# Optimization experiments

Hardware: AMD Instinct MI355X
Metric: run time of the kernel (lower is better)

## Reference

```python
import jax, jax.numpy as jnp
import numpy as np

OUT = 7      # roi_align output_size
RATIO = 2    # fixed sampling_ratio (torchvision default -1 is adaptive; fixed 2 used for jit-ability)
IMG = 518    # image size (DINOv2 patch 14 -> 37x37 feature grid)


def setup_inputs() -> dict:
    key = jax.random.key(0)
    ks = jax.random.split(key, 12)
    B, N, C, H, W = 4, 512, 256, 37, 37
    NUM_CLASSES = 91
    f0 = jax.random.normal(ks[0], (B, C, H, W), jnp.float32)
    f1 = jax.random.normal(ks[1], (B, C, H, W), jnp.float32)
    f2 = jax.random.normal(ks[2], (B, C, H, W), jnp.float32)
    f3 = jax.random.normal(ks[3], (B, C, H, W), jnp.float32)
    # proposals in image coords so areas span all 4 level buckets (32^2..128^2+)
    cx = jax.random.uniform(ks[4], (B, N)) * IMG
    cy = jax.random.uniform(ks[5], (B, N)) * IMG
    bw = jax.random.uniform(ks[6], (B, N)) * 248.0 + 8.0
    bh = jax.random.uniform(ks[7], (B, N)) * 248.0 + 8.0
    x1 = jnp.maximum(cx - 0.5 * bw, 0.0)
    y1 = jnp.maximum(cy - 0.5 * bh, 0.0)
    x2 = jnp.minimum(cx + 0.5 * bw, float(IMG))
    y2 = jnp.minimum(cy + 0.5 * bh, float(IMG))
    proposals = jnp.stack([x1, y1, x2, y2], axis=-1)  # [B,N,4]
    D = C * OUT * OUT  # 12544
    w1 = jax.random.normal(ks[8], (D, 1024), jnp.float32) * 0.02
    b1 = jnp.zeros((1024,), jnp.float32)
    w2 = jax.random.normal(ks[9], (1024, 1024), jnp.float32) * 0.02
    b2 = jnp.zeros((1024,), jnp.float32)
    wc = jax.random.normal(ks[10], (1024, NUM_CLASSES), jnp.float32) * 0.02
    bc = jnp.zeros((NUM_CLASSES,), jnp.float32)
    wb = jax.random.normal(ks[11], (1024, 4), jnp.float32) * 0.02
    bb = jnp.zeros((4,), jnp.float32)
    return {"f0": f0, "f1": f1, "f2": f2, "f3": f3, "proposals": proposals,
            "w1": w1, "b1": b1, "w2": w2, "b2": b2,
            "wc": wc, "bc": bc, "wb": wb, "bb": bb}


def _multilevel_roi_align(f0, f1, f2, f3, proposals):
    B, C, H, W = f0.shape
    N = proposals.shape[1]
    P = OUT * RATIO * OUT * RATIO
    # levels stacked along spatial axis: [B, C, 4*H*W]
    feats_cat = jnp.stack([f0, f1, f2, f3], axis=2).reshape(B, C, 4 * H * W)
    bw = proposals[..., 2] - proposals[..., 0]
    bh = proposals[..., 3] - proposals[..., 1]
    area = bw * bh
    # area-based FPN level: <32^2->0, <64^2->1, <128^2->2, else 3
    lvl = ((area >= 32.0 ** 2).astype(jnp.int32)
           + (area >= 64.0 ** 2).astype(jnp.int32)
           + (area >= 128.0 ** 2).astype(jnp.int32))  # [B,N]
    # roi_align, spatial_scale=1.0, aligned=True
    x1 = proposals[..., 0] - 0.5
    y1 = proposals[..., 1] - 0.5
    bin_w = bw / OUT
    bin_h = bh / OUT
    offs = jnp.arange(OUT, dtype=jnp.float32)[:, None] + (jnp.arange(RATIO, dtype=jnp.float32) + 0.5)[None, :] / RATIO  # [7,2]
    ys = y1[..., None, None] + offs * bin_h[..., None, None]  # [B,N,7,2]
    xs = x1[..., None, None] + offs * bin_w[..., None, None]  # [B,N,7,2]
    y = ys[..., :, :, None, None]  # [B,N,7,2,1,1]
    x = xs[..., None, None, :, :]  # [B,N,1,1,7,2]
    valid = ((y >= -1.0) & (y <= H) & (x >= -1.0) & (x <= W)).astype(f0.dtype)
    yc = jnp.clip(y, 0.0, H - 1.0)
    xc = jnp.clip(x, 0.0, W - 1.0)
    y0f = jnp.floor(yc)
    x0f = jnp.floor(xc)
    y0 = y0f.astype(jnp.int32)
    x0 = x0f.astype(jnp.int32)
    y1i = jnp.minimum(y0 + 1, H - 1)
    x1i = jnp.minimum(x0 + 1, W - 1)
    ly = yc - y0f
    lx = xc - x0f
    hy = 1.0 - ly
    hx = 1.0 - lx
    base = (lvl * (H * W))[:, :, None, None, None, None]
    shp = (B, N, OUT, RATIO, OUT, RATIO)

    def gather(yi, xi):
        idx = jnp.broadcast_to(base + yi * W + xi, shp).reshape(B, N * P)
        return jax.vmap(lambda fb, ib: jnp.take(fb, ib, axis=1))(feats_cat, idx)  # [B,C,N*P]

    def wflat(w):
        return jnp.broadcast_to(w * valid, shp).reshape(B, 1, N * P)

    acc = (wflat(hy * hx) * gather(y0, x0)
           + wflat(hy * lx) * gather(y0, x1i)
           + wflat(ly * hx) * gather(y1i, x0)
           + wflat(ly * lx) * gather(y1i, x1i))
    roi = acc.reshape(B, C, N, OUT, RATIO, OUT, RATIO).sum(axis=(4, 6)) / (RATIO * RATIO)
    return roi.transpose(0, 2, 1, 3, 4)  # [B,N,C,7,7]


def reference(f0, f1, f2, f3, proposals, w1, b1, w2, b2, wc, bc, wb, bb):
    B, N = proposals.shape[0], proposals.shape[1]
    roi = _multilevel_roi_align(f0, f1, f2, f3, proposals)  # [B,N,C,7,7]
    flat = roi.reshape(B * N, -1)  # torch flatten order matches [C,7,7]
    h1 = jax.nn.relu(flat @ w1 + b1)
    h2 = jax.nn.relu(h1 @ w2 + b2)
    scores = (h2 @ wc + bc).reshape(B, N, -1)
    bbox_deltas = (h2 @ wb + bb).reshape(B, N, 4)
    return scores, bbox_deltas
```

## Files before the change

### kernel.cpp

```cpp
#include <hip/hip_runtime.h>
#include <hip/hip_bf16.h>
#include <stdint.h>

#define FH 37
#define FW 37
#define FC 256
#define NB 4
#define NP 512
#define BNT (NB*NP)
#define KDIM (FC*49)
#define HID 1024
#define NHEAD 95
#define CAP 256

typedef __bf16 bf16x8 __attribute__((ext_vector_type(8)));
typedef float  f32x4  __attribute__((ext_vector_type(4)));

__global__ __launch_bounds__(256) void k_init(uint4* __restrict__ Ahi4,
                                              uint4* __restrict__ Alo4,
                                              int* __restrict__ count,
                                              float* __restrict__ h2c_raw) {
  int bid = blockIdx.x;
  if (bid < 1568) {
    int i = bid * 256 + threadIdx.x;
    uint4 z = {0, 0, 0, 0};
    Ahi4[i] = z;
    Alo4[i] = z;
  } else {
    int t = threadIdx.x;
    #pragma unroll
    for (int j = 0; j < 4; ++j) h2c_raw[t + j * 256] = 0.f;
    if (t == 0) *count = 0;
  }
}

__global__ __launch_bounds__(256) void k_transpose(const float* __restrict__ f0,
                                                   const float* __restrict__ f1,
                                                   const float* __restrict__ f2,
                                                   const float* __restrict__ f3,
                                                   float* __restrict__ ft) {
  __shared__ float tile[32][33];
  int bl = blockIdx.z;
  int b = bl >> 2, l = bl & 3;
  const float* src = (l == 0 ? f0 : l == 1 ? f1 : l == 2 ? f2 : f3) + (size_t)b * FC * FH * FW;
  int yx0 = blockIdx.x * 32;
  int c0  = blockIdx.y * 32;
  int tx = threadIdx.x;
  int ty = threadIdx.y;
  #pragma unroll
  for (int i = 0; i < 32; i += 8) {
    int c  = c0 + ty + i;
    int yx = yx0 + tx;
    float v = (yx < FH * FW) ? src[(size_t)c * (FH * FW) + yx] : 0.f;
    tile[ty + i][tx] = v;
  }
  __syncthreads();
  #pragma unroll
  for (int i = 0; i < 32; i += 8) {
    int yx = yx0 + ty + i;
    int c  = c0 + tx;
    if (yx < FH * FW)
      ft[((size_t)bl * (FH * FW) + yx) * FC + c] = tile[tx][ty + i];
  }
}

__global__ __launch_bounds__(256) void k_compact(const float* __restrict__ props,
                                                 int* __restrict__ count,
                                                 int* __restrict__ list) {
  int bn = blockIdx.x * 256 + threadIdx.x;
  float px1 = props[(size_t)bn * 4 + 0];
  float py1 = props[(size_t)bn * 4 + 1];
  float px2 = props[(size_t)bn * 4 + 2];
  float py2 = props[(size_t)bn * 4 + 3];
  float bw = px2 - px1, bh = py2 - py1;
  float X1 = px1 - 0.5f, Y1 = py1 - 0.5f;
  float binw = bw * (1.f / 7.f), binh = bh * (1.f / 7.f);
  float sy0 = Y1 + ((float)0 * 0.5f + 0.25f) * binh;
  float sx0 = X1 + ((float)0 * 0.5f + 0.25f) * binw;
  bool active = (sy0 <= 37.f) && (sx0 <= 37.f);
  if (active) {
    int s = atomicAdd(count, 1);
    if (s < CAP) list[s] = bn;
  }
}

__global__ __launch_bounds__(256) void k_roi(const float* __restrict__ ft,
                                             const float* __restrict__ props,
                                             const int* __restrict__ count,
                                             const int* __restrict__ list,
                                             __hip_bfloat16* __restrict__ Ahi,
                                             __hip_bfloat16* __restrict__ Alo) {
  __shared__ int   s_idx[28][4];
  __shared__ float s_w[28][4];
  int s = blockIdx.x;
  int cnt = min(*count, CAP);
  if (s >= cnt) return;
  int bn = list[s];
  int b = bn >> 9;
  int oy = blockIdx.y;
  int t = threadIdx.x;
  if (t < 28) {
    float px1 = props[(size_t)bn * 4 + 0];
    float py1 = props[(size_t)bn * 4 + 1];
    float px2 = props[(size_t)bn * 4 + 2];
    float py2 = props[(size_t)bn * 4 + 3];
    float bw = px2 - px1, bh = py2 - py1;
    float area = bw * bh;
    int lvl = (area >= 1024.f) + (area >= 4096.f) + (area >= 16384.f);
    float X1 = px1 - 0.5f, Y1 = py1 - 0.5f;
    float binw = bw * (1.f / 7.f), binh = bh * (1.f / 7.f);
    int ry = t / 14, ix = t % 14;
    int iy = oy * 2 + ry;
    float sy = Y1 + ((float)iy * 0.5f + 0.25f) * binh;
    float sx = X1 + ((float)ix * 0.5f + 0.25f) * binw;
    float valid = (sy >= -1.f && sy <= 37.f && sx >= -1.f && sx <= 37.f) ? 0.25f : 0.f;
    float yc = fminf(fmaxf(sy, 0.f), 36.f);
    float xc = fminf(fmaxf(sx, 0.f), 36.f);
    float y0f = floorf(yc), x0f = floorf(xc);
    int y0 = (int)y0f, x0 = (int)x0f;
    int y1i = min(y0 + 1, 36), x1i = min(x0 + 1, 36);
    float ly = yc - y0f, lx = xc - x0f;
    float hy = 1.f - ly, hx = 1.f - lx;
    int base = ((b * 4 + lvl) * (FH * FW)) * FC;
    s_idx[t][0] = base + (y0 * FW + x0) * FC;
    s_idx[t][1] = base + (y0 * FW + x1i) * FC;
    s_idx[t][2] = base + (y1i * FW + x0) * FC;
    s_idx[t][3] = base + (y1i * FW + x1i) * FC;
    s_w[t][0] = hy * hx * valid;
    s_w[t][1] = hy * lx * valid;
    s_w[t][2] = ly * hx * valid;
    s_w[t][3] = ly * lx * valid;
  }
  __syncthreads();
  int c = t;
  size_t outbase = (size_t)s * KDIM;
  for (int ox = 0; ox < 7; ++ox) {
    float acc = 0.f;
    #pragma unroll
    for (int ry = 0; ry < 2; ++ry) {
      #pragma unroll
      for (int rx = 0; rx < 2; ++rx) {
        int sp = ry * 14 + ox * 2 + rx;
        #pragma unroll
        for (int tap = 0; tap < 4; ++tap) {
          float wt = s_w[sp][tap];
          if (wt != 0.f) acc += wt * ft[s_idx[sp][tap] + c];
        }
      }
    }
    int p = oy * 7 + ox;
    __hip_bfloat16 h = __float2bfloat16(acc);
    Ahi[outbase + p * FC + c] = h;
    Alo[outbase + p * FC + c] = __float2bfloat16(acc - __bfloat162float(h));
  }
}

__global__ __launch_bounds__(256) void k_w1(const float* __restrict__ w1,
                                            __hip_bfloat16* __restrict__ Whi,
                                            __hip_bfloat16* __restrict__ Wlo) {
  __shared__ float tile[64][65];
  int p  = blockIdx.x;
  int c0 = blockIdx.y * 64;
  int n0 = blockIdx.z * 64;
  int t = threadIdx.x;
  int tl = t & 63, th = t >> 6;
  #pragma unroll
  for (int i = 0; i < 16; ++i) {
    int r = i * 4 + th;
    tile[r][tl] = w1[((size_t)(c0 + r) * 49 + p) * HID + n0 + tl];
  }
  __syncthreads();
  #pragma unroll
  for (int i = 0; i < 16; ++i) {
    int r = i * 4 + th;
    float v = tile[tl][r];
    __hip_bfloat16 h = __float2bfloat16(v);
    size_t o = (size_t)(n0 + r) * KDIM + p * FC + c0 + tl;
    Whi[o] = h;
    Wlo[o] = __float2bfloat16(v - __bfloat162float(h));
  }
}

__global__ __launch_bounds__(256) void k_w2(const float* __restrict__ w2,
                                            __hip_bfloat16* __restrict__ Whi,
                                            __hip_bfloat16* __restrict__ Wlo) {
  __shared__ float tile[64][65];
  int k0 = blockIdx.x * 64;
  int n0 = blockIdx.y * 64;
  int t = threadIdx.x;
  int tl = t & 63, th = t >> 6;
  #pragma unroll
  for (int i = 0; i < 16; ++i) {
    int r = i * 4 + th;
    tile[r][tl] = w2[(size_t)(k0 + r) * HID + n0 + tl];
  }
  __syncthreads();
  #pragma unroll
  for (int i = 0; i < 16; ++i) {
    int r = i * 4 + th;
    float v = tile[tl][r];
    __hip_bfloat16 h = __float2bfloat16(v);
    size_t o = (size_t)(n0 + r) * HID + k0 + tl;
    Whi[o] = h;
    Wlo[o] = __float2bfloat16(v - __bfloat162float(h));
  }
}

__global__ __launch_bounds__(256) void k_wcb(const float* __restrict__ wc,
                                             const float* __restrict__ bc,
                                             const float* __restrict__ wb,
                                             const float* __restrict__ bb,
                                             float* __restrict__ wcbT,
                                             float* __restrict__ bcb) {
  int j = blockIdx.x;
  int t = threadIdx.x;
  for (int k = t; k < HID; k += 256) {
    float v = (j < 91) ? wc[(size_t)k * 91 + j] : wb[(size_t)k * 4 + (j - 91)];
    wcbT[(size_t)j * HID + k] = v;
  }
  if (t == 0) bcb[j] = (j < 91) ? bc[j] : bb[j - 91];
}

__global__ __launch_bounds__(256) void k_h2c(const float* __restrict__ w2,
                                             const float* __restrict__ b1,
                                             float* __restrict__ h2c_raw) {
  int n = blockIdx.x * 256 + threadIdx.x;
  int k0 = blockIdx.y * 64;
  float acc = 0.f;
  for (int k = k0; k < k0 + 64; ++k) {
    float h = fmaxf(b1[k], 0.f);
    acc += h * w2[(size_t)k * HID + n];
  }
  atomicAdd(&h2c_raw[n], acc);
}

__global__ __launch_bounds__(256) void k_outc(const float* __restrict__ h2c_raw,
                                              const float* __restrict__ b2,
                                              const float* __restrict__ wcbT,
                                              const float* __restrict__ bcb,
                                              float* __restrict__ outc) {
  __shared__ float red[4];
  int j = blockIdx.x;
  int t = threadIdx.x;
  float acc = 0.f;
  for (int n = t; n < HID; n += 256) {
    float h = fmaxf(b2[n] + h2c_raw[n], 0.f);
    acc += h * wcbT[(size_t)j * HID + n];
  }
  #pragma unroll
  for (int o = 32; o; o >>= 1) acc += __shfl_down(acc, o, 64);
  if ((t & 63) == 0) red[t >> 6] = acc;
  __syncthreads();
  if (t == 0) outc[j] = bcb[j] + red[0] + red[1] + red[2] + red[3];
}

__global__ __launch_bounds__(256) void k_fill(const float* __restrict__ outc,
                                              float* __restrict__ out) {
  int i = blockIdx.x * 256 + threadIdx.x;
  const int SC = BNT * 91;
  if (i < SC) out[i] = outc[i % 91];
  else {
    int r = i - SC;
    if (r < BNT * 4) out[SC + r] = outc[91 + (r & 3)];
  }
}

__global__ __launch_bounds__(256) void k_gemm(const __hip_bfloat16* __restrict__ Ahi,
                                              const __hip_bfloat16* __restrict__ Alo,
                                              const __hip_bfloat16* __restrict__ Bhi,
                                              const __hip_bfloat16* __restrict__ Blo,
                                              float* __restrict__ part,
                                              const int* __restrict__ countPtr,
                                              int Mm, int Kt, int Nn, int kChunk) {
  int cnt = min(*countPtr, CAP);
  if (blockIdx.x * 128 >= cnt) return;
  __shared__ char lds[32768];
  int t = threadIdx.x, lane = t & 63, wave = t >> 6;
  int m0 = blockIdx.x * 128, n0 = blockIdx.y * 128;
  int kStart = blockIdx.z * kChunk;

  f32x4 acc[4][4];
  #pragma unroll
  for (int m = 0; m < 4; ++m)
    #pragma unroll
    for (int n = 0; n < 4; ++n)
      acc[m][n] = (f32x4){0.f, 0.f, 0.f, 0.f};

  const __hip_bfloat16* srcs[4] = {
      Ahi + (size_t)m0 * Kt, Alo + (size_t)m0 * Kt,
      Bhi + (size_t)n0 * Kt, Blo + (size_t)n0 * Kt};

  int wm = (wave >> 1) * 64, wn = (wave & 1) * 64;
  int rsel = lane & 15;
  int ksel = (lane >> 4) * 16;

  for (int kk = 0; kk < kChunk; kk += 32) {
    int k0 = kStart + kk;
    #pragma unroll
    for (int tile = 0; tile < 4; ++tile) {
      #pragma unroll
      for (int i = 0; i < 2; ++i) {
        int seg = wave * 2 + i;
        int idx = seg * 64 + lane;
        int row = idx >> 2, col = idx & 3;
        const char* g = (const char*)(srcs[tile] + (size_t)row * Kt + k0 + col * 8);
        char* l = lds + tile * 8192 + seg * 1024;
        __builtin_amdgcn_global_load_lds((const unsigned int __attribute__((address_space(1)))*)g,
                                         (unsigned int __attribute__((address_space(3)))*)l,
                                         16, 0, 0);
      }
    }
    __syncthreads();
    bf16x8 ah[4], al_[4], bh[4], bl_[4];
    #pragma unroll
    for (int m = 0; m < 4; ++m) {
      int off = (wm + m * 16 + rsel) * 64 + ksel;
      ah[m]  = *(const bf16x8*)(lds + off);
      al_[m] = *(const bf16x8*)(lds + 8192 + off);
    }
    #pragma unroll
    for (int n = 0; n < 4; ++n) {
      int off = (wn + n * 16 + rsel) * 64 + ksel;
      bh[n]  = *(const bf16x8*)(lds + 16384 + off);
      bl_[n] = *(const bf16x8*)(lds + 24576 + off);
    }
    #pragma unroll
    for (int m = 0; m < 4; ++m)
      #pragma unroll
      for (int n = 0; n < 4; ++n) {
        acc[m][n] = __builtin_amdgcn_mfma_f32_16x16x32_bf16(ah[m],  bh[n],  acc[m][n], 0, 0, 0);
        acc[m][n] = __builtin_amdgcn_mfma_f32_16x16x32_bf16(ah[m],  bl_[n], acc[m][n], 0, 0, 0);
        acc[m][n] = __builtin_amdgcn_mfma_f32_16x16x32_bf16(al_[m], bh[n],  acc[m][n], 0, 0, 0);
      }
    __syncthreads();
  }

  float* pbase = part + (size_t)blockIdx.z * Mm * Nn;
  #pragma unroll
  for (int m = 0; m < 4; ++m)
    #pragma unroll
    for (int n = 0; n < 4; ++n) {
      int row = m0 + wm + m * 16 + (lane >> 4) * 4;
      int col = n0 + wn + n * 16 + (lane & 15);
      #pragma unroll
      for (int r = 0; r < 4; ++r)
        pbase[(size_t)(row + r) * Nn + col] = acc[m][n][r];
    }
}

template <bool SPLIT_OUT>
__global__ __launch_bounds__(256) void k_reduce(const float* __restrict__ part,
                                                const float* __restrict__ bias,
                                                int Mm, int Nn, int S,
                                                __hip_bfloat16* __restrict__ Hhi,
                                                __hip_bfloat16* __restrict__ Hlo,
                                                float* __restrict__ Hf) {
  size_t i = (size_t)blockIdx.x * 256 + threadIdx.x;
  size_t tot = (size_t)Mm * Nn;
  if (i >= tot) return;
  int col = (int)(i % Nn);
  float a = bias[col];
  for (int s = 0; s < S; ++s) a += part[(size_t)s * tot + i];
  a = fmaxf(a, 0.f);
  if (SPLIT_OUT) {
    __hip_bfloat16 h = __float2bfloat16(a);
    Hhi[i] = h;
    Hlo[i] = __float2bfloat16(a - __bfloat162float(h));
  } else {
    Hf[i] = a;
  }
}

__global__ __launch_bounds__(128) void k_head(const float* __restrict__ h2,
                                              const float* __restrict__ wcbT,
                                              const float* __restrict__ bcb,
                                              const int* __restrict__ count,
                                              const int* __restrict__ list,
                                              float* __restrict__ out) {
  __shared__ float row[HID];
  int s = blockIdx.x;
  int cnt = min(*count, CAP);
  if (s >= cnt) return;
  int bn = list[s];
  int t = threadIdx.x;
  const float4* hr = (const float4*)(h2 + (size_t)s * HID);
  for (int i = t; i < HID / 4; i += 128) ((float4*)row)[i] = hr[i];
  __syncthreads();
  if (t < NHEAD) {
    const float4* w4 = (const float4*)(wcbT + (size_t)t * HID);
    const float4* r4 = (const float4*)row;
    float acc = bcb[t];
    #pragma unroll 4
    for (int k = 0; k < HID / 4; ++k) {
      float4 a = r4[k], b = w4[k];
      acc += a.x * b.x + a.y * b.y + a.z * b.z + a.w * b.w;
    }
    if (t < 91) out[(size_t)bn * 91 + t] = acc;
    else        out[(size_t)BNT * 91 + (size_t)bn * 4 + (t - 91)] = acc;
  }
}

extern "C" void kernel_launch(void* const* d_in, const int* in_sizes, int n_in,
                              void* d_out, int out_size, void* d_ws, size_t ws_size,
                              hipStream_t stream) {
  const float* f0    = (const float*)d_in[0];
  const float* f1    = (const float*)d_in[1];
  const float* f2    = (const float*)d_in[2];
  const float* f3    = (const float*)d_in[3];
  const float* props = (const float*)d_in[4];
  const float* w1    = (const float*)d_in[5];
  const float* b1    = (const float*)d_in[6];
  const float* w2    = (const float*)d_in[7];
  const float* b2    = (const float*)d_in[8];
  const float* wc    = (const float*)d_in[9];
  const float* bc    = (const float*)d_in[10];
  const float* wb    = (const float*)d_in[11];
  const float* bb    = (const float*)d_in[12];
  float* out = (float*)d_out;

  char* ws = (char*)d_ws;
  size_t off = 0;
  auto alloc = [&](size_t bytes) -> char* {
    char* p = ws + off;
    off += (bytes + 255) & ~(size_t)255;
    return p;
  };
  float*          ft    = (float*)         alloc((size_t)16 * FH * FW * FC * 4);
  __hip_bfloat16* Ahi   = (__hip_bfloat16*)alloc((size_t)CAP * KDIM * 2);
  __hip_bfloat16* Alo   = (__hip_bfloat16*)alloc((size_t)CAP * KDIM * 2);
  __hip_bfloat16* W1hi  = (__hip_bfloat16*)alloc((size_t)HID * KDIM * 2);
  __hip_bfloat16* W1lo  = (__hip_bfloat16*)alloc((size_t)HID * KDIM * 2);
  __hip_bfloat16* W2hi  = (__hip_bfloat16*)alloc((size_t)HID * HID * 2);
  __hip_bfloat16* W2lo  = (__hip_bfloat16*)alloc((size_t)HID * HID * 2);
  float*          wcbT  = (float*)         alloc((size_t)96 * HID * 4);
  float*          bcb   = (float*)         alloc(96 * 4);
  float*          part  = (float*)         alloc((size_t)14 * CAP * HID * 4);
  __hip_bfloat16* H1hi  = (__hip_bfloat16*)alloc((size_t)CAP * HID * 2);
  __hip_bfloat16* H1lo  = (__hip_bfloat16*)alloc((size_t)CAP * HID * 2);
  float*          h2    = (float*)         alloc((size_t)CAP * HID * 4);
  int*            count = (int*)           alloc(256);
  int*            list  = (int*)           alloc(CAP * 4);
  float*          h2cr  = (float*)         alloc(HID * 4);
  float*          outc  = (float*)         alloc(NHEAD * 4);
  (void)ws_size; (void)in_sizes; (void)n_in; (void)out_size;

  k_init<<<1569, 256, 0, stream>>>((uint4*)Ahi, (uint4*)Alo, count, h2cr);
  k_transpose<<<dim3(43, 8, 16), dim3(32, 8), 0, stream>>>(f0, f1, f2, f3, ft);
  k_compact<<<8, 256, 0, stream>>>(props, count, list);
  k_roi<<<dim3(CAP, 7), 256, 0, stream>>>(ft, props, count, list, Ahi, Alo);
  k_w1<<<dim3(49, 4, 16), 256, 0, stream>>>(w1, W1hi, W1lo);
  k_w2<<<dim3(16, 16), 256, 0, stream>>>(w2, W2hi, W2lo);
  k_wcb<<<NHEAD, 256, 0, stream>>>(wc, bc, wb, bb, wcbT, bcb);
  k_h2c<<<dim3(4, 16), 256, 0, stream>>>(w2, b1, h2cr);
  k_outc<<<NHEAD, 256, 0, stream>>>(h2cr, b2, wcbT, bcb, outc);
  k_fill<<<760, 256, 0, stream>>>(outc, out);

  k_gemm<<<dim3(CAP / 128, 8, 14), 256, 0, stream>>>(Ahi, Alo, W1hi, W1lo, part, count,
                                                     CAP, KDIM, HID, 896);
  k_reduce<true><<<(CAP * HID + 255) / 256, 256, 0, stream>>>(part, b1, CAP, HID, 14,
                                                              H1hi, H1lo, nullptr);
  k_gemm<<<dim3(CAP / 128, 8, 4), 256, 0, stream>>>(H1hi, H1lo, W2hi, W2lo, part, count,
                                                    CAP, HID, HID, 256);
  k_reduce<false><<<(CAP * HID + 255) / 256, 256, 0, stream>>>(part, b2, CAP, HID, 4,
                                                               nullptr, nullptr, h2);
  k_head<<<CAP, 128, 0, stream>>>(h2, wcbT, bcb, count, list, out);
}
```

Before: 286.3 us.

## Fuse fp32 weight bf16 hi/lo split into a double-buffered GEMM

Removes the per-call preprocessing kernels that converted w1, w2 and the head weights into transposed bf16 hi/lo copies. The GEMM now reads fp32 weights directly, with a K-index reorder for w1's layout, and splits them into hi/lo on the fly into swizzled LDS. It also double-buffers A and B with K=64 stages and doubles the split-K factor. The head and constant-path kernels now read the original weights, the A-buffer zeroing kernel is replaced by a small memset, and the reduces skip rows beyond the valid count. This trades extra conversion ALU work inside the GEMM, and a larger LDS footprint at one block per CU, for eliminating roughly a hundred megabytes of weight write and re-read traffic.

```diff
diff --git a/kernel.cpp b/kernel.cpp
--- a/kernel.cpp
+++ b/kernel.cpp
@@ -15,24 +15,6 @@
 
 typedef __bf16 bf16x8 __attribute__((ext_vector_type(8)));
 typedef float  f32x4  __attribute__((ext_vector_type(4)));
-
-__global__ __launch_bounds__(256) void k_init(uint4* __restrict__ Ahi4,
-                                              uint4* __restrict__ Alo4,
-                                              int* __restrict__ count,
-                                              float* __restrict__ h2c_raw) {
-  int bid = blockIdx.x;
-  if (bid < 1568) {
-    int i = bid * 256 + threadIdx.x;
-    uint4 z = {0, 0, 0, 0};
-    Ahi4[i] = z;
-    Alo4[i] = z;
-  } else {
-    int t = threadIdx.x;
-    #pragma unroll
-    for (int j = 0; j < 4; ++j) h2c_raw[t + j * 256] = 0.f;
-    if (t == 0) *count = 0;
-  }
-}
 
 __global__ __launch_bounds__(256) void k_transpose(const float* __restrict__ f0,
                                                    const float* __restrict__ f1,
@@ -155,129 +137,24 @@
   }
 }
 
-__global__ __launch_bounds__(256) void k_w1(const float* __restrict__ w1,
-                                            __hip_bfloat16* __restrict__ Whi,
-                                            __hip_bfloat16* __restrict__ Wlo) {
-  __shared__ float tile[64][65];
-  int p  = blockIdx.x;
-  int c0 = blockIdx.y * 64;
-  int n0 = blockIdx.z * 64;
-  int t = threadIdx.x;
-  int tl = t & 63, th = t >> 6;
-  #pragma unroll
-  for (int i = 0; i < 16; ++i) {
-    int r = i * 4 + th;
-    tile[r][tl] = w1[((size_t)(c0 + r) * 49 + p) * HID + n0 + tl];
-  }
-  __syncthreads();
-  #pragma unroll
-  for (int i = 0; i < 16; ++i) {
-    int r = i * 4 + th;
-    float v = tile[tl][r];
-    __hip_bfloat16 h = __float2bfloat16(v);
-    size_t o = (size_t)(n0 + r) * KDIM + p * FC + c0 + tl;
-    Whi[o] = h;
-    Wlo[o] = __float2bfloat16(v - __bfloat162float(h));
-  }
-}
-
-__global__ __launch_bounds__(256) void k_w2(const float* __restrict__ w2,
-                                            __hip_bfloat16* __restrict__ Whi,
-                                            __hip_bfloat16* __restrict__ Wlo) {
-  __shared__ float tile[64][65];
-  int k0 = blockIdx.x * 64;
-  int n0 = blockIdx.y * 64;
-  int t = threadIdx.x;
-  int tl = t & 63, th = t >> 6;
-  #pragma unroll
-  for (int i = 0; i < 16; ++i) {
-    int r = i * 4 + th;
-    tile[r][tl] = w2[(size_t)(k0 + r) * HID + n0 + tl];
-  }
-  __syncthreads();
-  #pragma unroll
-  for (int i = 0; i < 16; ++i) {
-    int r = i * 4 + th;
-    float v = tile[tl][r];
-    __hip_bfloat16 h = __float2bfloat16(v);
-    size_t o = (size_t)(n0 + r) * HID + k0 + tl;
-    Whi[o] = h;
-    Wlo[o] = __float2bfloat16(v - __bfloat162float(h));
-  }
-}
-
-__global__ __launch_bounds__(256) void k_wcb(const float* __restrict__ wc,
-                                             const float* __restrict__ bc,
-                                             const float* __restrict__ wb,
-                                             const float* __restrict__ bb,
-                                             float* __restrict__ wcbT,
-                                             float* __restrict__ bcb) {
-  int j = blockIdx.x;
-  int t = threadIdx.x;
-  for (int k = t; k < HID; k += 256) {
-    float v = (j < 91) ? wc[(size_t)k * 91 + j] : wb[(size_t)k * 4 + (j - 91)];
-    wcbT[(size_t)j * HID + k] = v;
-  }
-  if (t == 0) bcb[j] = (j < 91) ? bc[j] : bb[j - 91];
-}
-
-__global__ __launch_bounds__(256) void k_h2c(const float* __restrict__ w2,
-                                             const float* __restrict__ b1,
-                                             float* __restrict__ h2c_raw) {
-  int n = blockIdx.x * 256 + threadIdx.x;
-  int k0 = blockIdx.y * 64;
-  float acc = 0.f;
-  for (int k = k0; k < k0 + 64; ++k) {
-    float h = fmaxf(b1[k], 0.f);
-    acc += h * w2[(size_t)k * HID + n];
-  }
-  atomicAdd(&h2c_raw[n], acc);
-}
-
-__global__ __launch_bounds__(256) void k_outc(const float* __restrict__ h2c_raw,
-                                              const float* __restrict__ b2,
-                                              const float* __restrict__ wcbT,
-                                              const float* __restrict__ bcb,
-                                              float* __restrict__ outc) {
-  __shared__ float red[4];
-  int j = blockIdx.x;
-  int t = threadIdx.x;
-  float acc = 0.f;
-  for (int n = t; n < HID; n += 256) {
-    float h = fmaxf(b2[n] + h2c_raw[n], 0.f);
-    acc += h * wcbT[(size_t)j * HID + n];
-  }
-  #pragma unroll
-  for (int o = 32; o; o >>= 1) acc += __shfl_down(acc, o, 64);
-  if ((t & 63) == 0) red[t >> 6] = acc;
-  __syncthreads();
-  if (t == 0) outc[j] = bcb[j] + red[0] + red[1] + red[2] + red[3];
-}
-
-__global__ __launch_bounds__(256) void k_fill(const float* __restrict__ outc,
-                                              float* __restrict__ out) {
-  int i = blockIdx.x * 256 + threadIdx.x;
-  const int SC = BNT * 91;
-  if (i < SC) out[i] = outc[i % 91];
-  else {
-    int r = i - SC;
-    if (r < BNT * 4) out[SC + r] = outc[91 + (r & 3)];
-  }
-}
-
-__global__ __launch_bounds__(256) void k_gemm(const __hip_bfloat16* __restrict__ Ahi,
-                                              const __hip_bfloat16* __restrict__ Alo,
-                                              const __hip_bfloat16* __restrict__ Bhi,
-                                              const __hip_bfloat16* __restrict__ Blo,
-                                              float* __restrict__ part,
-                                              const int* __restrict__ countPtr,
-                                              int Mm, int Kt, int Nn, int kChunk) {
+__global__ __launch_bounds__(256, 1) void k_gemm_fused(
+    const __hip_bfloat16* __restrict__ Ahi,
+    const __hip_bfloat16* __restrict__ Alo,
+    const float* __restrict__ Wf,
+    float* __restrict__ part,
+    const int* __restrict__ countPtr,
+    int Kt, int kChunk, int reorder) {
   int cnt = min(*countPtr, CAP);
-  if (blockIdx.x * 128 >= cnt) return;
-  __shared__ char lds[32768];
-  int t = threadIdx.x, lane = t & 63, wave = t >> 6;
-  int m0 = blockIdx.x * 128, n0 = blockIdx.y * 128;
-  int kStart = blockIdx.z * kChunk;
+  if ((int)blockIdx.x * 128 >= cnt) return;
+  __shared__ __align__(16) char lds[131072];
+  const int t = threadIdx.x, lane = t & 63, wave = t >> 6;
+  const int m0 = blockIdx.x * 128, n0 = blockIdx.y * 128;
+  const int kStart = blockIdx.z * kChunk;
+  const int niters = kChunk >> 6;
+
+  const int bn = t & 127;
+  const int bkq = t >> 7;
+  const size_t rs = reorder ? (size_t)49 * HID : (size_t)HID;
 
   f32x4 acc[4][4];
   #pragma unroll
@@ -286,79 +163,132 @@
     for (int n = 0; n < 4; ++n)
       acc[m][n] = (f32x4){0.f, 0.f, 0.f, 0.f};
 
-  const __hip_bfloat16* srcs[4] = {
-      Ahi + (size_t)m0 * Kt, Alo + (size_t)m0 * Kt,
-      Bhi + (size_t)n0 * Kt, Blo + (size_t)n0 * Kt};
-
-  int wm = (wave >> 1) * 64, wn = (wave & 1) * 64;
-  int rsel = lane & 15;
-  int ksel = (lane >> 4) * 16;
-
-  for (int kk = 0; kk < kChunk; kk += 32) {
-    int k0 = kStart + kk;
-    #pragma unroll
-    for (int tile = 0; tile < 4; ++tile) {
-      #pragma unroll
-      for (int i = 0; i < 2; ++i) {
-        int seg = wave * 2 + i;
-        int idx = seg * 64 + lane;
-        int row = idx >> 2, col = idx & 3;
-        const char* g = (const char*)(srcs[tile] + (size_t)row * Kt + k0 + col * 8);
-        char* l = lds + tile * 8192 + seg * 1024;
+  float v[32];
+
+  auto stageA = [&](int buf, int k0) {
+    #pragma unroll
+    for (int pl = 0; pl < 2; ++pl) {
+      const __hip_bfloat16* src = pl ? Alo : Ahi;
+      #pragma unroll
+      for (int i = 0; i < 4; ++i) {
+        int seg = wave * 4 + i;
+        int row = seg * 8 + (lane >> 3);
+        int chunk = (lane & 7) ^ (row & 7);
+        const char* g = (const char*)(src + (size_t)(m0 + row) * Kt + k0 + chunk * 8);
+        char* l = lds + buf * 65536 + pl * 16384 + seg * 1024;
         __builtin_amdgcn_global_load_lds((const unsigned int __attribute__((address_space(1)))*)g,
                                          (unsigned int __attribute__((address_space(3)))*)l,
                                          16, 0, 0);
       }
     }
+  };
+
+  auto stageBload = [&](int k0) {
+    size_t rb = reorder ? (size_t)((k0 & 255) * 49 + (k0 >> 8)) : (size_t)k0;
+    const float* p = Wf + rb * HID + (size_t)bkq * 32 * rs + n0 + bn;
+    #pragma unroll
+    for (int j = 0; j < 32; ++j) v[j] = p[(size_t)j * rs];
+  };
+
+  auto stageBwrite = [&](int buf) {
+    char* bh = lds + buf * 65536 + 32768;
+    char* bl = lds + buf * 65536 + 49152;
+    #pragma unroll
+    for (int s = 0; s < 4; ++s) {
+      bf16x8 hv, lv;
+      #pragma unroll
+      for (int e = 0; e < 8; ++e) {
+        float f = v[s * 8 + e];
+        __hip_bfloat16 h = __float2bfloat16(f);
+        float fr = f - __bfloat162float(h);
+        __hip_bfloat16 l2 = __float2bfloat16(fr);
+        hv[e] = *reinterpret_cast<__bf16*>(&h);
+        lv[e] = *reinterpret_cast<__bf16*>(&l2);
+      }
+      int off = bn * 128 + (((bkq * 4 + s) ^ (bn & 7)) << 4);
+      *(bf16x8*)(bh + off) = hv;
+      *(bf16x8*)(bl + off) = lv;
+    }
+  };
+
+  const int wm = (wave >> 1) * 64, wn = (wave & 1) * 64;
+  const int rsel = lane & 15, q = lane >> 4;
+
+  auto compute = [&](int buf) {
+    const char* base = lds + buf * 65536;
+    #pragma unroll
+    for (int kk = 0; kk < 2; ++kk) {
+      bf16x8 ah[4], al_[4], bh[4], bl_[4];
+      #pragma unroll
+      for (int m = 0; m < 4; ++m) {
+        int row = wm + m * 16 + rsel;
+        int off = row * 128 + (((kk * 4 + q) ^ (row & 7)) << 4);
+        ah[m]  = *(const bf16x8*)(base + off);
+        al_[m] = *(const bf16x8*)(base + 16384 + off);
+      }
+      #pragma unroll
+      for (int n = 0; n < 4; ++n) {
+        int col = wn + n * 16 + rsel;
+        int off = col * 128 + (((kk * 4 + q) ^ (col & 7)) << 4);
+        bh[n]  = *(const bf16x8*)(base + 32768 + off);
+        bl_[n] = *(const bf16x8*)(base + 49152 + off);
+      }
+      #pragma unroll
+      for (int m = 0; m < 4; ++m)
+        #pragma unroll
+        for (int n = 0; n < 4; ++n) {
+          acc[m][n] = __builtin_amdgcn_mfma_f32_16x16x32_bf16(ah[m],  bh[n],  acc[m][n], 0, 0, 0);
+          acc[m][n] = __builtin_amdgcn_mfma_f32_16x16x32_bf16(ah[m],  bl_[n], acc[m][n], 0, 0, 0);
+          acc[m][n] = __builtin_amdgcn_mfma_f32_16x16x32_bf16(al_[m], bh[n],  acc[m][n], 0, 0, 0);
+        }
+    }
+  };
+
+  stageBload(kStart);
+  stageA(0, kStart);
+  stageBwrite(0);
+  __syncthreads();
+
+  int cur = 0;
+  for (int it = 0; it < niters; ++it) {
+    int k1 = kStart + (it + 1) * 64;
+    bool havenext = (it + 1 < niters);
+    if (havenext) {
+      stageBload(k1);
+      stageA(cur ^ 1, k1);
+    }
+    compute(cur);
+    if (havenext) stageBwrite(cur ^ 1);
     __syncthreads();
-    bf16x8 ah[4], al_[4], bh[4], bl_[4];
-    #pragma unroll
-    for (int m = 0; m < 4; ++m) {
-      int off = (wm + m * 16 + rsel) * 64 + ksel;
-      ah[m]  = *(const bf16x8*)(lds + off);
-      al_[m] = *(const bf16x8*)(lds + 8192 + off);
-    }
-    #pragma unroll
-    for (int n = 0; n < 4; ++n) {
-      int off = (wn + n * 16 + rsel) * 64 + ksel;
-      bh[n]  = *(const bf16x8*)(lds + 16384 + off);
-      bl_[n] = *(const bf16x8*)(lds + 24576 + off);
-    }
-    #pragma unroll
-    for (int m = 0; m < 4; ++m)
-      #pragma unroll
-      for (int n = 0; n < 4; ++n) {
-        acc[m][n] = __builtin_amdgcn_mfma_f32_16x16x32_bf16(ah[m],  bh[n],  acc[m][n], 0, 0, 0);
-        acc[m][n] = __builtin_amdgcn_mfma_f32_16x16x32_bf16(ah[m],  bl_[n], acc[m][n], 0, 0, 0);
-        acc[m][n] = __builtin_amdgcn_mfma_f32_16x16x32_bf16(al_[m], bh[n],  acc[m][n], 0, 0, 0);
-      }
-    __syncthreads();
-  }
-
-  float* pbase = part + (size_t)blockIdx.z * Mm * Nn;
+    cur ^= 1;
+  }
+
+  float* pbase = part + (size_t)blockIdx.z * (CAP * HID);
   #pragma unroll
   for (int m = 0; m < 4; ++m)
     #pragma unroll
     for (int n = 0; n < 4; ++n) {
-      int row = m0 + wm + m * 16 + (lane >> 4) * 4;
-      int col = n0 + wn + n * 16 + (lane & 15);
+      int row = m0 + wm + m * 16 + q * 4;
+      int col = n0 + wn + n * 16 + rsel;
       #pragma unroll
       for (int r = 0; r < 4; ++r)
-        pbase[(size_t)(row + r) * Nn + col] = acc[m][n][r];
+        pbase[(size_t)(row + r) * HID + col] = acc[m][n][r];
     }
 }
 
 template <bool SPLIT_OUT>
 __global__ __launch_bounds__(256) void k_reduce(const float* __restrict__ part,
                                                 const float* __restrict__ bias,
-                                                int Mm, int Nn, int S,
+                                                const int* __restrict__ countPtr,
+                                                int S,
                                                 __hip_bfloat16* __restrict__ Hhi,
                                                 __hip_bfloat16* __restrict__ Hlo,
                                                 float* __restrict__ Hf) {
+  int cnt = min(*countPtr, CAP);
+  if ((int)(blockIdx.x >> 2) >= cnt) return;
   size_t i = (size_t)blockIdx.x * 256 + threadIdx.x;
-  size_t tot = (size_t)Mm * Nn;
-  if (i >= tot) return;
-  int col = (int)(i % Nn);
+  const size_t tot = (size_t)CAP * HID;
+  int col = (int)(i & (HID - 1));
   float a = bias[col];
   for (int s = 0; s < S; ++s) a += part[(size_t)s * tot + i];
   a = fmaxf(a, 0.f);
@@ -371,9 +301,59 @@
   }
 }
 
+__global__ __launch_bounds__(256) void k_h2c(const float* __restrict__ w2,
+                                             const float* __restrict__ b1,
+                                             float* __restrict__ h2cr) {
+  int n = blockIdx.x * 256 + threadIdx.x;
+  int k0 = blockIdx.y * 128;
+  float acc = 0.f;
+  for (int k = k0; k < k0 + 128; ++k)
+    acc += fmaxf(b1[k], 0.f) * w2[(size_t)k * HID + n];
+  atomicAdd(&h2cr[n], acc);
+}
+
+__global__ __launch_bounds__(256) void k_outc(const float* __restrict__ h2cr,
+                                              const float* __restrict__ b2,
+                                              const float* __restrict__ wc,
+                                              const float* __restrict__ bc,
+                                              const float* __restrict__ wb,
+                                              const float* __restrict__ bb,
+                                              float* __restrict__ outc) {
+  __shared__ float red[4];
+  int j = blockIdx.x;
+  int t = threadIdx.x;
+  float acc = 0.f;
+  for (int n = t; n < HID; n += 256) {
+    float h = fmaxf(b2[n] + h2cr[n], 0.f);
+    float w = (j < 91) ? wc[(size_t)n * 91 + j] : wb[(size_t)n * 4 + (j - 91)];
+    acc += h * w;
+  }
+  #pragma unroll
+  for (int o = 32; o; o >>= 1) acc += __shfl_down(acc, o, 64);
+  if ((t & 63) == 0) red[t >> 6] = acc;
+  __syncthreads();
+  if (t == 0) {
+    float bj = (j < 91) ? bc[j] : bb[j - 91];
+    outc[j] = bj + red[0] + red[1] + red[2] + red[3];
+  }
+}
+
+__global__ __launch_bounds__(256) void k_fill(const float* __restrict__ outc,
+                                              float* __restrict__ out) {
+  int i = blockIdx.x * 256 + threadIdx.x;
+  const int SC = BNT * 91;
+  if (i < SC) out[i] = outc[i % 91];
+  else {
+    int r = i - SC;
+    if (r < BNT * 4) out[SC + r] = outc[91 + (r & 3)];
+  }
+}
+
 __global__ __launch_bounds__(128) void k_head(const float* __restrict__ h2,
-                                              const float* __restrict__ wcbT,
-                                              const float* __restrict__ bcb,
+                                              const float* __restrict__ wc,
+                                              const float* __restrict__ bc,
+                                              const float* __restrict__ wb,
+                                              const float* __restrict__ bb,
                                               const int* __restrict__ count,
                                               const int* __restrict__ list,
                                               float* __restrict__ out) {
@@ -387,16 +367,14 @@
   for (int i = t; i < HID / 4; i += 128) ((float4*)row)[i] = hr[i];
   __syncthreads();
   if (t < NHEAD) {
-    const float4* w4 = (const float4*)(wcbT + (size_t)t * HID);
-    const float4* r4 = (const float4*)row;
-    float acc = bcb[t];
-    #pragma unroll 4
-    for (int k = 0; k < HID / 4; ++k) {
-      float4 a = r4[k], b = w4[k];
-      acc += a.x * b.x + a.y * b.y + a.z * b.z + a.w * b.w;
-    }
-    if (t < 91) out[(size_t)bn * 91 + t] = acc;
-    else        out[(size_t)BNT * 91 + (size_t)bn * 4 + (t - 91)] = acc;
+    float acc = (t < 91) ? bc[t] : bb[t - 91];
+    if (t < 91) {
+      for (int k = 0; k < HID; ++k) acc += row[k] * wc[(size_t)k * 91 + t];
+      out[(size_t)bn * 91 + t] = acc;
+    } else {
+      for (int k = 0; k < HID; ++k) acc += row[k] * wb[(size_t)k * 4 + (t - 91)];
+      out[(size_t)BNT * 91 + (size_t)bn * 4 + (t - 91)] = acc;
+    }
   }
 }
 
@@ -428,40 +406,33 @@
   float*          ft    = (float*)         alloc((size_t)16 * FH * FW * FC * 4);
   __hip_bfloat16* Ahi   = (__hip_bfloat16*)alloc((size_t)CAP * KDIM * 2);
   __hip_bfloat16* Alo   = (__hip_bfloat16*)alloc((size_t)CAP * KDIM * 2);
-  __hip_bfloat16* W1hi  = (__hip_bfloat16*)alloc((size_t)HID * KDIM * 2);
-  __hip_bfloat16* W1lo  = (__hip_bfloat16*)alloc((size_t)HID * KDIM * 2);
-  __hip_bfloat16* W2hi  = (__hip_bfloat16*)alloc((size_t)HID * HID * 2);
-  __hip_bfloat16* W2lo  = (__hip_bfloat16*)alloc((size_t)HID * HID * 2);
-  float*          wcbT  = (float*)         alloc((size_t)96 * HID * 4);
-  float*          bcb   = (float*)         alloc(96 * 4);
-  float*          part  = (float*)         alloc((size_t)14 * CAP * HID * 4);
+  float*          part  = (float*)         alloc((size_t)28 * CAP * HID * 4);
   __hip_bfloat16* H1hi  = (__hip_bfloat16*)alloc((size_t)CAP * HID * 2);
   __hip_bfloat16* H1lo  = (__hip_bfloat16*)alloc((size_t)CAP * HID * 2);
   float*          h2    = (float*)         alloc((size_t)CAP * HID * 4);
+  float*          h2cr  = (float*)         alloc(HID * 4);
   int*            count = (int*)           alloc(256);
   int*            list  = (int*)           alloc(CAP * 4);
-  float*          h2cr  = (float*)         alloc(HID * 4);
   float*          outc  = (float*)         alloc(NHEAD * 4);
   (void)ws_size; (void)in_sizes; (void)n_in; (void)out_size;
 
-  k_init<<<1569, 256, 0, stream>>>((uint4*)Ahi, (uint4*)Alo, count, h2cr);
+  hipMemsetAsync(h2cr, 0, HID * 4 + 256, stream);
+
   k_transpose<<<dim3(43, 8, 16), dim3(32, 8), 0, stream>>>(f0, f1, f2, f3, ft);
   k_compact<<<8, 256, 0, stream>>>(props, count, list);
   k_roi<<<dim3(CAP, 7), 256, 0, stream>>>(ft, props, count, list, Ahi, Alo);
-  k_w1<<<dim3(49, 4, 16), 256, 0, stream>>>(w1, W1hi, W1lo);
-  k_w2<<<dim3(16, 16), 256, 0, stream>>>(w2, W2hi, W2lo);
-  k_wcb<<<NHEAD, 256, 0, stream>>>(wc, bc, wb, bb, wcbT, bcb);
-  k_h2c<<<dim3(4, 16), 256, 0, stream>>>(w2, b1, h2cr);
-  k_outc<<<NHEAD, 256, 0, stream>>>(h2cr, b2, wcbT, bcb, outc);
+
+  k_h2c<<<dim3(4, 8), 256, 0, stream>>>(w2, b1, h2cr);
+  k_outc<<<NHEAD, 256, 0, stream>>>(h2cr, b2, wc, bc, wb, bb, outc);
   k_fill<<<760, 256, 0, stream>>>(outc, out);
 
-  k_gemm<<<dim3(CAP / 128, 8, 14), 256, 0, stream>>>(Ahi, Alo, W1hi, W1lo, part, count,
-                                                     CAP, KDIM, HID, 896);
-  k_reduce<true><<<(CAP * HID + 255) / 256, 256, 0, stream>>>(part, b1, CAP, HID, 14,
-                                                              H1hi, H1lo, nullptr);
-  k_gemm<<<dim3(CAP / 128, 8, 4), 256, 0, stream>>>(H1hi, H1lo, W2hi, W2lo, part, count,
-                                                    CAP, HID, HID, 256);
-  k_reduce<false><<<(CAP * HID + 255) / 256, 256, 0, stream>>>(part, b2, CAP, HID, 4,
-                                                               nullptr, nullptr, h2);
-  k_head<<<CAP, 128, 0, stream>>>(h2, wcbT, bcb, count, list, out);
-}
+  k_gemm_fused<<<dim3(CAP / 128, 8, 28), 256, 0, stream>>>(Ahi, Alo, w1, part, count,
+                                                           KDIM, 448, 1);
+  k_reduce<true><<<CAP * HID / 256, 256, 0, stream>>>(part, b1, count, 28,
+                                                      H1hi, H1lo, nullptr);
+  k_gemm_fused<<<dim3(CAP / 128, 8, 8), 256, 0, stream>>>(H1hi, H1lo, w2, part, count,
+                                                          HID, 128, 0);
+  k_reduce<false><<<CAP * HID / 256, 256, 0, stream>>>(part, b2, count, 8,
+                                                       nullptr, nullptr, h2);
+  k_head<<<CAP, 128, 0, stream>>>(h2, wc, bc, wb, bb, count, list, out);
+}
```

Result: faster. 262.6 us (-8.3%).
